# Performance work log

Measured on AMD Instinct MI355X. Metric: run time of the kernel, lower is better.

The kernel has to match this reference:

```python
import jax, jax.numpy as jnp
import numpy as np

USER_NUM = 100000
ITEM_NUM = 100000  # padding index; table has ITEM_NUM+1 rows
D = 64
B = 4096
L = 200
NEG_WEIGHT = 0.1


def setup_inputs() -> dict:
    key = jax.random.key(0)
    k1, k2, k3, k4, k5 = jax.random.split(key, 5)
    uids = jax.random.randint(k1, (B,), 0, USER_NUM, dtype=jnp.int64 if jax.config.jax_enable_x64 else jnp.int32)
    pos_iids = jax.random.randint(k2, (B, L), 0, ITEM_NUM + 1, dtype=jnp.int64 if jax.config.jax_enable_x64 else jnp.int32)
    user_W = jax.random.normal(k3, (USER_NUM, D), dtype=jnp.float32) * 0.1
    item_W = jax.random.normal(k4, (ITEM_NUM + 1, D), dtype=jnp.float32) * 0.1
    h = jnp.full((D, 1), 0.01, dtype=jnp.float32)  # reset_para: constant 0.01
    return {"uids": uids, "pos_iids": pos_iids, "user_W": user_W, "item_W": item_W, "h": h}


def reference(uids, pos_iids, user_W, item_W, h):
    u_emb = user_W[uids]                      # [B, D] (dropout p=0 -> identity)
    pos_embs = item_W[pos_iids]               # [B, L, D]
    mask = (pos_iids != ITEM_NUM).astype(u_emb.dtype)  # padding id masked out
    pos_embs = pos_embs * mask[:, :, None]
    # hpq[b,l] = sum_d u[b,d] * pos[b,l,d] * h[d]
    hpq = jnp.einsum('bd,bld,d->bl', u_emb, pos_embs, h[:, 0])
    pos_data_loss = jnp.sum((1.0 - NEG_WEIGHT) * jnp.square(hpq) - 2.0 * hpq)
    # part_1/part_2 in torch are sums of per-row outer products == Gram matrices
    part_1 = item_W.T @ item_W                # [D, D]
    part_2 = u_emb.T @ u_emb                  # [D, D]
    part_3 = h @ h.T                          # [D, D]
    all_data_loss = jnp.sum(part_1 * part_2 * part_3)
    return NEG_WEIGHT * all_data_loss + pos_data_loss
```

## Files before the change

kernel.cpp:

```cpp
#include <hip/hip_runtime.h>

#define D 64
#define ITEM_PAD 100000
#define LSEQ 200
#define BATCH 4096
#define NEG_W 0.1f
#define NBI 512
#define NBU 64
#define GSZ (D * D)

#define BFT_FLOATS 3200032
#define PITEM_OFF  ((size_t)BFT_FLOATS)
#define PUSER_OFF  (PITEM_OFF + (size_t)NBI * GSZ)
#define POS_OFF    (PUSER_OFF + (size_t)NBU * GSZ)
#define GDOT_OFF   (POS_OFF + BATCH)

__device__ __forceinline__ unsigned short f2bf_rne(float x) {
    unsigned u = __builtin_bit_cast(unsigned, x);
    return (unsigned short)((u + 0x7fffu + ((u >> 16) & 1u)) >> 16);
}
__device__ __forceinline__ float bf_lo(unsigned u) {
    return __builtin_bit_cast(float, u << 16);
}
__device__ __forceinline__ float bf_hi(unsigned u) {
    return __builtin_bit_cast(float, u & 0xffff0000u);
}

__global__ void gram_convert(const int* __restrict__ uids,
                             const float* __restrict__ user_W,
                             const float* __restrict__ item_W,
                             float* __restrict__ ws) {
    __shared__ float smem[32 * D];
    const int bid = blockIdx.x;
    const int t   = threadIdx.x;

    const bool item = (bid < NBI);
    const float* __restrict__ W = item ? item_W : user_W;
    const int* __restrict__ idx = item ? nullptr : uids;
    const int nrows  = item ? (ITEM_PAD + 1) : BATCH;
    const int stride = item ? NBI : NBU;
    const int b0     = item ? bid : bid - NBI;
    float* __restrict__ out =
        ws + (item ? PITEM_OFF + (size_t)b0 * GSZ : PUSER_OFF + (size_t)b0 * GSZ);
    unsigned short* __restrict__ bft = (unsigned short*)ws;

    const int ti = t >> 4;
    const int tj = t & 15;
    float acc[4][4] = {{0.f,0.f,0.f,0.f},{0.f,0.f,0.f,0.f},
                       {0.f,0.f,0.f,0.f},{0.f,0.f,0.f,0.f}};

    const int nchunks = (nrows + 31) >> 5;

    float4 va = make_float4(0.f,0.f,0.f,0.f), vb = va;
    int c = b0;
    if (c < nchunks) {
        const int ra = (c << 5) + ti, rb = ra + 16;
        if (ra < nrows) {
            const int sa = idx ? idx[ra] : ra;
            va = *(const float4*)(W + (size_t)sa * D + tj * 4);
        }
        if (rb < nrows) {
            const int sb = idx ? idx[rb] : rb;
            vb = *(const float4*)(W + (size_t)sb * D + tj * 4);
        }
    }

    while (c < nchunks) {
        __syncthreads();
        *(float4*)(smem + ti * D + tj * 4)        = va;
        *(float4*)(smem + (ti + 16) * D + tj * 4) = vb;

        if (item) {
            const int ra = (c << 5) + ti, rb = ra + 16;
            if (ra < nrows) {
                ushort4 s4 = { f2bf_rne(va.x), f2bf_rne(va.y),
                               f2bf_rne(va.z), f2bf_rne(va.w) };
                *(ushort4*)(bft + (size_t)ra * D + tj * 4) = s4;
            }
            if (rb < nrows) {
                ushort4 s4 = { f2bf_rne(vb.x), f2bf_rne(vb.y),
                               f2bf_rne(vb.z), f2bf_rne(vb.w) };
                *(ushort4*)(bft + (size_t)rb * D + tj * 4) = s4;
            }
        }
        __syncthreads();

        const int cn = c + stride;
        va = make_float4(0.f,0.f,0.f,0.f); vb = va;
        if (cn < nchunks) {
            const int ra = (cn << 5) + ti, rb = ra + 16;
            if (ra < nrows) {
                const int sa = idx ? idx[ra] : ra;
                va = *(const float4*)(W + (size_t)sa * D + tj * 4);
            }
            if (rb < nrows) {
                const int sb = idx ? idx[rb] : rb;
                vb = *(const float4*)(W + (size_t)sb * D + tj * 4);
            }
        }

        #pragma unroll
        for (int r2 = 0; r2 < 32; ++r2) {
            float xi[4], xj[4];
            *(float4*)xi = *(const float4*)(smem + r2 * D + ti * 4);
            *(float4*)xj = *(const float4*)(smem + r2 * D + tj * 4);
            #pragma unroll
            for (int a = 0; a < 4; ++a)
                #pragma unroll
                for (int b2 = 0; b2 < 4; ++b2)
                    acc[a][b2] += xi[a] * xj[b2];
        }
        c = cn;
    }
    #pragma unroll
    for (int a = 0; a < 4; ++a)
        *(float4*)(out + (ti * 4 + a) * D + tj * 4) = *(const float4*)acc[a];
}

__global__ void pos_and_reduce(const int* __restrict__ uids,
                               const int* __restrict__ pos_iids,
                               const float* __restrict__ user_W,
                               const float* __restrict__ h,
                               float* __restrict__ ws) {
    const int bid = blockIdx.x;
    const int t   = threadIdx.x;
    const int lane = t & 63;
    const int wave = t >> 6;

    if (bid < BATCH) {
        __shared__ float uh[D];
        __shared__ int   sidx[LSEQ];
        __shared__ float red[4];
        const int b = bid;
        const unsigned short* __restrict__ bft = (const unsigned short*)ws;

        if (t < LSEQ) sidx[t] = pos_iids[(size_t)b * LSEQ + t];
        if (t >= 192) {
            const int j = t - 192;
            uh[j] = user_W[(size_t)uids[b] * D + j] * h[j];
        }
        __syncthreads();

        const int p    = lane >> 3;
        const int q    = lane & 7;
        const int base = wave * 8 + p;

        float u8[8];
        *(float4*)(u8 + 0) = *(const float4*)(uh + q * 8);
        *(float4*)(u8 + 4) = *(const float4*)(uh + q * 8 + 4);

        int ids[7];
        #pragma unroll
        for (int k = 0; k < 7; ++k) {
            const int l = base + 32 * k;
            ids[k] = (l < LSEQ) ? sidx[l] : ITEM_PAD;
        }
        uint4 rows[7];
        #pragma unroll
        for (int k = 0; k < 7; ++k) {
            uint4 v = make_uint4(0u, 0u, 0u, 0u);
            if (ids[k] != ITEM_PAD)
                v = *(const uint4*)(bft + (size_t)ids[k] * D + q * 8);
            rows[k] = v;
        }

        float local = 0.f;
        #pragma unroll
        for (int k = 0; k < 7; ++k) {
            const uint4 v = rows[k];
            float s = bf_lo(v.x)*u8[0] + bf_hi(v.x)*u8[1]
                    + bf_lo(v.y)*u8[2] + bf_hi(v.y)*u8[3]
                    + bf_lo(v.z)*u8[4] + bf_hi(v.z)*u8[5]
                    + bf_lo(v.w)*u8[6] + bf_hi(v.w)*u8[7];
            s += __shfl_xor(s, 1);
            s += __shfl_xor(s, 2);
            s += __shfl_xor(s, 4);
            if (q == 0)
                local += (1.0f - NEG_W) * s * s - 2.0f * s;
        }
        local += __shfl_xor(local, 1);
        local += __shfl_xor(local, 2);
        local += __shfl_xor(local, 4);
        local += __shfl_xor(local, 8);
        local += __shfl_xor(local, 16);
        local += __shfl_xor(local, 32);
        if (lane == 0) red[wave] = local;
        __syncthreads();
        if (t == 0)
            ws[POS_OFF + b] = red[0] + red[1] + red[2] + red[3];
    } else {
        __shared__ float rI[4][16];
        __shared__ float rU[4][16];
        const int bb = bid - BATCH;
        const int kk = t & 15;
        const int ps = t >> 4;
        const int k  = bb * 16 + kk;

        float si = 0.f, su = 0.f;
        #pragma unroll 8
        for (int p = ps; p < NBI; p += 16) si += ws[PITEM_OFF + (size_t)p * GSZ + k];
        #pragma unroll
        for (int p = ps; p < NBU; p += 16) su += ws[PUSER_OFF + (size_t)p * GSZ + k];

        si += __shfl_xor(si, 16); si += __shfl_xor(si, 32);
        su += __shfl_xor(su, 16); su += __shfl_xor(su, 32);
        if (lane < 16) { rI[wave][kk] = si; rU[wave][kk] = su; }
        __syncthreads();

        if (wave == 0) {
            float c = 0.f;
            if (t < 16) {
                const float Gi = rI[0][t] + rI[1][t] + rI[2][t] + rI[3][t];
                const float Gu = rU[0][t] + rU[1][t] + rU[2][t] + rU[3][t];
                const int kg = bb * 16 + t;
                const int i = kg >> 6, j = kg & 63;
                c = NEG_W * Gi * Gu * h[i] * h[j];
            }
            c += __shfl_xor(c, 1);
            c += __shfl_xor(c, 2);
            c += __shfl_xor(c, 4);
            c += __shfl_xor(c, 8);
            if (lane == 0) ws[GDOT_OFF + bb] = c;
        }
    }
}

__global__ void final_sum(const float* __restrict__ ws, float* __restrict__ out) {
    __shared__ float red[4];
    const int t = threadIdx.x;
    float s = 0.f;
    #pragma unroll
    for (int k = 0; k < 17; ++k)
        s += ws[POS_OFF + t + k * 256];
    s += __shfl_xor(s, 1);
    s += __shfl_xor(s, 2);
    s += __shfl_xor(s, 4);
    s += __shfl_xor(s, 8);
    s += __shfl_xor(s, 16);
    s += __shfl_xor(s, 32);
    const int lane = t & 63, wave = t >> 6;
    if (lane == 0) red[wave] = s;
    __syncthreads();
    if (t == 0) out[0] = red[0] + red[1] + red[2] + red[3];
}

extern "C" void kernel_launch(void* const* d_in, const int* in_sizes, int n_in,
                              void* d_out, int out_size, void* d_ws, size_t ws_size,
                              hipStream_t stream) {
    const int*   uids     = (const int*)d_in[0];
    const int*   pos_iids = (const int*)d_in[1];
    const float* user_W   = (const float*)d_in[2];
    const float* item_W   = (const float*)d_in[3];
    const float* h        = (const float*)d_in[4];
    float* out = (float*)d_out;
    float* ws  = (float*)d_ws;

    gram_convert<<<NBI + NBU, 256, 0, stream>>>(uids, user_W, item_W, ws);
    pos_and_reduce<<<BATCH + 256, 256, 0, stream>>>(uids, pos_iids, user_W, h, ws);
    final_sum<<<1, 256, 0, stream>>>(ws, out);
}
```

Before: 121.9 us.

## Compute Gram matrices with bf16 MFMA on larger chunks instead of FP32 FMA

The Gram-matrix kernel now stages 128-row chunks as bf16 in padded LDS and accumulates the 64x64 outer-product sums with 16x16x32 bf16 MFMA instructions across four waves. Per-wave partial results are reduced through shared memory before being written, and the block counts are halved to match the larger chunks. This replaces scalar FP32 FMAs with matrix-core work. It lowers the precision of the Gram products to bf16 inputs and adds a serialized cross-wave reduction at the end. The output layout must also be consistent with what the reduce kernel expects.

```diff
diff --git a/kernel.cpp b/kernel.cpp
--- a/kernel.cpp
+++ b/kernel.cpp
@@ -2,12 +2,15 @@
 
 #define D 64
 #define ITEM_PAD 100000
+#define NROW_I (ITEM_PAD + 1)
 #define LSEQ 200
 #define BATCH 4096
 #define NEG_W 0.1f
-#define NBI 512
-#define NBU 64
+#define CH 128
+#define NBI 256
+#define NBU 32
 #define GSZ (D * D)
+#define LDS_P 66
 
 #define BFT_FLOATS 3200032
 #define PITEM_OFF  ((size_t)BFT_FLOATS)
@@ -15,6 +18,9 @@
 #define POS_OFF    (PUSER_OFF + (size_t)NBU * GSZ)
 #define GDOT_OFF   (POS_OFF + BATCH)
 
+typedef short  bf16x8 __attribute__((ext_vector_type(8)));
+typedef float  f32x4  __attribute__((ext_vector_type(4)));
+
 __device__ __forceinline__ unsigned short f2bf_rne(float x) {
     unsigned u = __builtin_bit_cast(unsigned, x);
     return (unsigned short)((u + 0x7fffu + ((u >> 16) & 1u)) >> 16);
@@ -26,95 +32,130 @@
     return __builtin_bit_cast(float, u & 0xffff0000u);
 }
 
-__global__ void gram_convert(const int* __restrict__ uids,
-                             const float* __restrict__ user_W,
-                             const float* __restrict__ item_W,
-                             float* __restrict__ ws) {
-    __shared__ float smem[32 * D];
-    const int bid = blockIdx.x;
-    const int t   = threadIdx.x;
-
+__global__ void __launch_bounds__(256)
+gram_convert(const int* __restrict__ uids,
+             const float* __restrict__ user_W,
+             const float* __restrict__ item_W,
+             float* __restrict__ ws) {
+    __shared__ __align__(16) unsigned char smraw[CH * LDS_P * 2];
+    ushort* sm16 = (ushort*)smraw;
+    float*  smF  = (float*)smraw;
+
+    const int bid  = blockIdx.x;
+    const int t    = threadIdx.x;
     const bool item = (bid < NBI);
+    const int b0   = item ? bid : bid - NBI;
     const float* __restrict__ W = item ? item_W : user_W;
-    const int* __restrict__ idx = item ? nullptr : uids;
-    const int nrows  = item ? (ITEM_PAD + 1) : BATCH;
+    const int nrows  = item ? NROW_I : BATCH;
     const int stride = item ? NBI : NBU;
-    const int b0     = item ? bid : bid - NBI;
-    float* __restrict__ out =
-        ws + (item ? PITEM_OFF + (size_t)b0 * GSZ : PUSER_OFF + (size_t)b0 * GSZ);
-    unsigned short* __restrict__ bft = (unsigned short*)ws;
-
-    const int ti = t >> 4;
-    const int tj = t & 15;
-    float acc[4][4] = {{0.f,0.f,0.f,0.f},{0.f,0.f,0.f,0.f},
-                       {0.f,0.f,0.f,0.f},{0.f,0.f,0.f,0.f}};
-
-    const int nchunks = (nrows + 31) >> 5;
-
-    float4 va = make_float4(0.f,0.f,0.f,0.f), vb = va;
+    const int nch    = (nrows + CH - 1) / CH;
+    ushort* __restrict__ bft = (ushort*)ws;
+    float*  __restrict__ out = ws + (item ? PITEM_OFF + (size_t)b0 * GSZ
+                                          : PUSER_OFF + (size_t)b0 * GSZ);
+
+    const int lane = t & 63;
+    const int wv   = t >> 6;
+    const int rl   = t >> 4;
+    const int c4   = t & 15;
+
+    f32x4 acc[4][4];
+    #pragma unroll
+    for (int a = 0; a < 4; ++a)
+        #pragma unroll
+        for (int b = 0; b < 4; ++b)
+            #pragma unroll
+            for (int r = 0; r < 4; ++r)
+                acc[a][b][r] = 0.f;
+
+    float4 v[8];
     int c = b0;
-    if (c < nchunks) {
-        const int ra = (c << 5) + ti, rb = ra + 16;
-        if (ra < nrows) {
-            const int sa = idx ? idx[ra] : ra;
-            va = *(const float4*)(W + (size_t)sa * D + tj * 4);
-        }
-        if (rb < nrows) {
-            const int sb = idx ? idx[rb] : rb;
-            vb = *(const float4*)(W + (size_t)sb * D + tj * 4);
+    if (c < nch) {
+        #pragma unroll
+        for (int i = 0; i < 8; ++i) {
+            const int r = c * CH + rl + 16 * i;
+            v[i] = make_float4(0.f, 0.f, 0.f, 0.f);
+            if (r < nrows) {
+                const int src = item ? r : uids[r];
+                v[i] = *(const float4*)(W + (size_t)src * D + c4 * 4);
+            }
         }
     }
 
-    while (c < nchunks) {
-        __syncthreads();
-        *(float4*)(smem + ti * D + tj * 4)        = va;
-        *(float4*)(smem + (ti + 16) * D + tj * 4) = vb;
-
-        if (item) {
-            const int ra = (c << 5) + ti, rb = ra + 16;
-            if (ra < nrows) {
-                ushort4 s4 = { f2bf_rne(va.x), f2bf_rne(va.y),
-                               f2bf_rne(va.z), f2bf_rne(va.w) };
-                *(ushort4*)(bft + (size_t)ra * D + tj * 4) = s4;
+    while (c < nch) {
+        __syncthreads();
+        #pragma unroll
+        for (int i = 0; i < 8; ++i) {
+            const int rloc = rl + 16 * i;
+            ushort2 lo = { f2bf_rne(v[i].x), f2bf_rne(v[i].y) };
+            ushort2 hi = { f2bf_rne(v[i].z), f2bf_rne(v[i].w) };
+            *(ushort2*)(sm16 + rloc * LDS_P + c4 * 4)     = lo;
+            *(ushort2*)(sm16 + rloc * LDS_P + c4 * 4 + 2) = hi;
+            if (item) {
+                const int r = c * CH + rloc;
+                if (r < nrows) {
+                    ushort4 s4 = { lo.x, lo.y, hi.x, hi.y };
+                    *(ushort4*)(bft + (size_t)r * D + c4 * 4) = s4;
+                }
             }
-            if (rb < nrows) {
-                ushort4 s4 = { f2bf_rne(vb.x), f2bf_rne(vb.y),
-                               f2bf_rne(vb.z), f2bf_rne(vb.w) };
-                *(ushort4*)(bft + (size_t)rb * D + tj * 4) = s4;
+        }
+        __syncthreads();
+
+        const int cn = c + stride;
+        #pragma unroll
+        for (int i = 0; i < 8; ++i) {
+            const int r = cn * CH + rl + 16 * i;
+            float4 nv = make_float4(0.f, 0.f, 0.f, 0.f);
+            if (cn < nch && r < nrows) {
+                const int src = item ? r : uids[r];
+                nv = *(const float4*)(W + (size_t)src * D + c4 * 4);
             }
-        }
-        __syncthreads();
-
-        const int cn = c + stride;
-        va = make_float4(0.f,0.f,0.f,0.f); vb = va;
-        if (cn < nchunks) {
-            const int ra = (cn << 5) + ti, rb = ra + 16;
-            if (ra < nrows) {
-                const int sa = idx ? idx[ra] : ra;
-                va = *(const float4*)(W + (size_t)sa * D + tj * 4);
-            }
-            if (rb < nrows) {
-                const int sb = idx ? idx[rb] : rb;
-                vb = *(const float4*)(W + (size_t)sb * D + tj * 4);
-            }
-        }
-
-        #pragma unroll
-        for (int r2 = 0; r2 < 32; ++r2) {
-            float xi[4], xj[4];
-            *(float4*)xi = *(const float4*)(smem + r2 * D + ti * 4);
-            *(float4*)xj = *(const float4*)(smem + r2 * D + tj * 4);
+            v[i] = nv;
+        }
+
+        const int rbase = wv * 32 + (lane >> 4) * 8;
+        const int cl    = lane & 15;
+        bf16x8 fr[4];
+        #pragma unroll
+        for (int a = 0; a < 4; ++a)
             #pragma unroll
-            for (int a = 0; a < 4; ++a)
-                #pragma unroll
-                for (int b2 = 0; b2 < 4; ++b2)
-                    acc[a][b2] += xi[a] * xj[b2];
-        }
+            for (int e = 0; e < 8; ++e)
+                fr[a][e] = (short)sm16[(rbase + e) * LDS_P + a * 16 + cl];
+
+        #pragma unroll
+        for (int a = 0; a < 4; ++a)
+            #pragma unroll
+            for (int b = 0; b < 4; ++b)
+                acc[a][b] = __builtin_amdgcn_mfma_f32_16x16x32_bf16(
+                                fr[a], fr[b], acc[a][b], 0, 0, 0);
         c = cn;
     }
+
+    __syncthreads();
+#define ACC_WRITE()  { _Pragma("unroll") for (int a = 0; a < 4; ++a) \
+                       _Pragma("unroll") for (int b = 0; b < 4; ++b) \
+                       _Pragma("unroll") for (int r = 0; r < 4; ++r) \
+                         smF[(((a*4+b)*4)+r)*64 + lane] = acc[a][b][r]; }
+#define ACC_ADD()    { _Pragma("unroll") for (int a = 0; a < 4; ++a) \
+                       _Pragma("unroll") for (int b = 0; b < 4; ++b) \
+                       _Pragma("unroll") for (int r = 0; r < 4; ++r) \
+                         acc[a][b][r] += smF[(((a*4+b)*4)+r)*64 + lane]; }
+    if (wv == 1) ACC_WRITE();
+    __syncthreads();
+    if (wv == 0) ACC_ADD();
+    __syncthreads();
+    if (wv == 2) ACC_WRITE();
+    __syncthreads();
+    if (wv == 0) ACC_ADD();
+    __syncthreads();
+    if (wv == 3) ACC_WRITE();
+    __syncthreads();
+    if (wv == 0) { ACC_ADD(); ACC_WRITE(); }
+    __syncthreads();
+#undef ACC_WRITE
+#undef ACC_ADD
     #pragma unroll
-    for (int a = 0; a < 4; ++a)
-        *(float4*)(out + (ti * 4 + a) * D + tj * 4) = *(const float4*)acc[a];
+    for (int k = 0; k < 4; ++k)
+        *(float4*)(out + (t + k * 256) * 4) = *(const float4*)(smF + (t + k * 256) * 4);
 }
 
 __global__ void pos_and_reduce(const int* __restrict__ uids,
```

Result: no change. 121.7 us (-0.2%).
